# Optimization experiments

Hardware: AMD Instinct MI355X
Metric: run time of the kernel (lower is better)

The kernel has to match this reference:

```python
import jax, jax.numpy as jnp
import numpy as np

B, K, C, HEADS, R, N, FF = 8, 512, 256, 8, 4, 64, 1024
HT = 2 * R + 1  # rel-pos table side = 9


def layer_norm(x, g, b, eps=1e-5):
    mu = jnp.mean(x, axis=-1, keepdims=True)
    var = jnp.var(x, axis=-1, keepdims=True)
    return (x - mu) * jax.lax.rsqrt(var + eps) * g + b


def grid_sample_table(table, grid):
    """Bilinear grid_sample, align_corners=True, zeros padding.
    table: [heads, H, W] (batch-expanded in torch, identical per batch)
    grid:  [b, k, n, 2] in [-1, 1]  ->  out [b, heads, k, n]
    """
    heads, H, W = table.shape
    gx = (grid[..., 0] + 1.0) * 0.5 * (W - 1)
    gy = (grid[..., 1] + 1.0) * 0.5 * (H - 1)
    x0 = jnp.floor(gx); y0 = jnp.floor(gy)
    x1 = x0 + 1.0;      y1 = y0 + 1.0
    wx1 = gx - x0; wx0 = 1.0 - wx1
    wy1 = gy - y0; wy0 = 1.0 - wy1
    flat = table.reshape(heads, H * W)

    def corner(yi, xi, w):
        valid = (xi >= 0) & (xi <= W - 1) & (yi >= 0) & (yi <= H - 1)
        idx = (jnp.clip(yi, 0, H - 1) * W + jnp.clip(xi, 0, W - 1)).astype(jnp.int32)
        return flat[:, idx] * jnp.where(valid, w, 0.0)[None]  # [heads,b,k,n]

    out = (corner(y0, x0, wy0 * wx0) + corner(y0, x1, wy0 * wx1)
           + corner(y1, x0, wy1 * wx0) + corner(y1, x1, wy1 * wx1))
    return jnp.moveaxis(out, 0, 1)  # [b, heads, k, n]


def setup_inputs() -> dict:
    key = jax.random.key(0)
    ks = jax.random.split(key, 16)
    s = 1.0 / np.sqrt(C)
    inp = {
        "query": jax.random.normal(ks[0], (B, K, C), jnp.float32),
        "local_feat": jax.random.normal(ks[1], (B, C, K, N), jnp.float32),
        "local_spat": jax.random.uniform(ks[2], (B, K, N, 2), jnp.float32) * 2.0 - 1.0,
        # rel-pos table is zeros-initialized in torch; use small randn so it's non-trivial
        "rel_table": jax.random.normal(ks[3], (HEADS, HT, HT), jnp.float32) * 0.02,
        "Wq": jax.random.normal(ks[4], (C, C), jnp.float32) * s,
        "bq": jnp.zeros((C,), jnp.float32),
        "Wk": jax.random.normal(ks[5], (C, C), jnp.float32) * s,
        "bk": jnp.zeros((C,), jnp.float32),
        "Wv": jax.random.normal(ks[6], (C, C), jnp.float32) * s,
        "bv": jnp.zeros((C,), jnp.float32),
        "Wo": jax.random.normal(ks[7], (C, C), jnp.float32) * s,
        "bo": jnp.zeros((C,), jnp.float32),
        "ln1_g": jnp.ones((C,), jnp.float32),
        "ln1_b": jnp.zeros((C,), jnp.float32),
        "W1": jax.random.normal(ks[8], (C, FF), jnp.float32) * s,
        "b1": jnp.zeros((FF,), jnp.float32),
        "W2": jax.random.normal(ks[9], (FF, C), jnp.float32) * (1.0 / np.sqrt(FF)),
        "b2": jnp.zeros((C,), jnp.float32),
        "ln2_g": jnp.ones((C,), jnp.float32),
        "ln2_b": jnp.zeros((C,), jnp.float32),
    }
    return inp


def reference(query, local_feat, local_spat, rel_table, Wq, bq, Wk, bk, Wv, bv,
              Wo, bo, ln1_g, ln1_b, W1, b1, W2, b2, ln2_g, ln2_b):
    b, k, c = query.shape
    heads = rel_table.shape[0]
    d = c // heads
    n = local_feat.shape[-1]
    # spatial_score: grid_sample of rel-pos table at per-key offsets -> attention bias
    bias = grid_sample_table(rel_table, local_spat)      # [b, heads, k, n]
    bias = jnp.transpose(bias, (0, 2, 1, 3))             # [b, k, heads, n]
    # local bilateral attention (query attends to its n local samples)
    q = (query @ Wq + bq).reshape(b, k, heads, d)
    feats = jnp.transpose(local_feat, (0, 2, 3, 1))      # [b, k, n, c]
    Kp = (feats @ Wk + bk).reshape(b, k, n, heads, d)
    Vp = (feats @ Wv + bv).reshape(b, k, n, heads, d)
    scores = jnp.einsum('bkhd,bknhd->bkhn', q, Kp) / jnp.sqrt(jnp.float32(d)) + bias
    attn = jax.nn.softmax(scores, axis=-1)
    ctx = jnp.einsum('bkhn,bknhd->bkhd', attn, Vp).reshape(b, k, c)
    x = layer_norm(query + ctx @ Wo + bo, ln1_g, ln1_b)
    h = jax.nn.gelu(x @ W1 + b1) @ W2 + b2
    out = layer_norm(x + h, ln2_g, ln2_b)
    # num_local_scales == 1: stack+mean over scales is identity
    return out
```

## Files before the change

kernel.cpp:

```cpp
#include <hip/hip_runtime.h>
#include <hip/hip_bf16.h>

typedef __hip_bfloat16 bf16;
typedef __attribute__((ext_vector_type(8))) short short8;
typedef __attribute__((ext_vector_type(4))) float float4_;

#define DEV static __device__ __forceinline__

DEV float blo(unsigned w){ return __uint_as_float(w << 16); }
DEV float bhi(unsigned w){ return __uint_as_float(w & 0xffff0000u); }
DEV unsigned short f2bu(float x){ bf16 h = __float2bfloat16(x); unsigned short u; __builtin_memcpy(&u, &h, 2); return u; }
DEV unsigned pack2(float a, float b){ return (unsigned)f2bu(a) | ((unsigned)f2bu(b) << 16); }

DEV float gelu_tanh(float x){
  float z = 0.7978845608028654f * (x + 0.044715f * x * x * x);
  float th = 2.0f / (1.0f + __expf(-2.0f * z)) - 1.0f;
  return 0.5f * x * (1.0f + th);
}


__global__ __launch_bounds__(256) void k_prep(
    const float* __restrict__ query, const float* __restrict__ Wq,
    const float* __restrict__ Wk, const float* __restrict__ Wv,
    const float* __restrict__ Wo, const float* __restrict__ W1, const float* __restrict__ W2,
    const float* __restrict__ bq,
    bf16* __restrict__ query_bf, bf16* __restrict__ WqkT, float* __restrict__ bias_qk,
    bf16* __restrict__ WvP, bf16* __restrict__ WoT, bf16* __restrict__ W1T, bf16* __restrict__ W2T)
{
  __shared__ ushort ts[64][72];
  __shared__ float wkS[32];
  const int t = threadIdx.x;
  const int bx = blockIdx.x;

  if (bx < 144){
    const float* src; bf16* dst; int ldi, ldo, kt, nt;
    if (bx < 16)      { src = Wo; dst = WoT; ldi = 256;  ldo = 256;  kt = bx & 3;        nt = bx >> 2; }
    else if (bx < 80) { src = W1; dst = W1T; ldi = 1024; ldo = 256;  kt = (bx-16) & 3;   nt = (bx-16) >> 2; }
    else              { src = W2; dst = W2T; ldi = 256;  ldo = 1024; kt = (bx-80) & 15;  nt = (bx-80) >> 4; }
    int k0 = kt * 64, n0 = nt * 64;
    {
      int r = t >> 2, c0 = (t & 3) * 16;
      #pragma unroll
      for (int g = 0; g < 4; g++){
        float4 v = *(const float4*)&src[(size_t)(k0 + r)*ldi + n0 + c0 + g*4];
        ts[r][c0+g*4+0] = f2bu(v.x); ts[r][c0+g*4+1] = f2bu(v.y);
        ts[r][c0+g*4+2] = f2bu(v.z); ts[r][c0+g*4+3] = f2bu(v.w);
      }
    }
    __syncthreads();
    {
      int rr = t >> 2, cc0 = (t & 3) * 16;
      unsigned wbuf[8];
      #pragma unroll
      for (int j = 0; j < 8; j++)
        wbuf[j] = (unsigned)ts[cc0+2*j][rr] | ((unsigned)ts[cc0+2*j+1][rr] << 16);
      uint4* d = (uint4*)(dst + (size_t)(n0 + rr)*ldo + k0 + cc0);
      d[0] = make_uint4(wbuf[0], wbuf[1], wbuf[2], wbuf[3]);
      d[1] = make_uint4(wbuf[4], wbuf[5], wbuf[6], wbuf[7]);
    }
  } else if (bx < 176){
    int idx = bx - 144, h = idx >> 2, kt = idx & 3, k0 = kt * 64;
    {
      int r = t >> 2, d0 = (t & 3) * 8;
      #pragma unroll
      for (int g = 0; g < 2; g++){
        float4 v = *(const float4*)&Wv[(size_t)(k0 + r)*256 + h*32 + d0 + g*4];
        ts[r][d0+g*4+0] = f2bu(v.x); ts[r][d0+g*4+1] = f2bu(v.y);
        ts[r][d0+g*4+2] = f2bu(v.z); ts[r][d0+g*4+3] = f2bu(v.w);
      }
    }
    __syncthreads();
    {
      int d = t >> 3, cc0 = (t & 7) * 8;
      unsigned wbuf[4];
      #pragma unroll
      for (int j = 0; j < 4; j++)
        wbuf[j] = (unsigned)ts[cc0+2*j][d] | ((unsigned)ts[cc0+2*j+1][d] << 16);
      *(uint4*)(WvP + (size_t)h*8192 + (size_t)d*256 + k0 + cc0) =
          make_uint4(wbuf[0], wbuf[1], wbuf[2], wbuf[3]);
    }
  } else if (bx < 240){
    int off = (bx - 176) * 16384;
    #pragma unroll
    for (int g = 0; g < 16; g++){
      int i = off + g*1024 + t*4;
      float4 v = *(const float4*)&query[i];
      *(uint2*)(query_bf + i) = make_uint2(pack2(v.x, v.y), pack2(v.z, v.w));
    }
  } else {
    int idx = bx - 240, h = idx >> 8, c = idx & 255;
    if (t < 32) wkS[t] = Wk[(size_t)c*256 + h*32 + t];
    __syncthreads();
    float acc = 0.f;
    const float* wq = Wq + (size_t)t*256 + h*32;
    #pragma unroll
    for (int d = 0; d < 32; d++) acc += wq[d] * wkS[d];
    WqkT[(size_t)(h*256 + c)*256 + t] = __float2bfloat16(acc);
    if (t == 0){
      float bacc = 0.f;
      #pragma unroll
      for (int d = 0; d < 32; d++) bacc += bq[h*32 + d] * wkS[d];
      bias_qk[h*256 + c] = bacc;
    }
  }
}

template<int KDIM, int NT, int EPI>
__global__ __launch_bounds__(256) void k_gemm(
    const bf16* __restrict__ A, int lda, int acolH,
    const bf16* __restrict__ BT, int btH,
    const float* __restrict__ bias,
    bf16* __restrict__ Cb, int ldc, int ncolH)
{
  constexpr int KB = (KDIM >= 64) ? 64 : 32;
  constexpr int LP = KB + 8;
  constexpr int ASEG = KB / 8;
  __shared__ short As[64][LP];
  __shared__ short Bs[NT][LP];

  const int t = threadIdx.x;
  const int w = t >> 6, l = t & 63, lm = l & 15, lq = l >> 4;
  const int m0 = blockIdx.x * 64;
  const int h = blockIdx.z;
  const size_t acol = (size_t)h * acolH;
  const bf16* Bt = BT + (size_t)h * btH + (size_t)(blockIdx.y * NT) * KDIM;
  const int ncol = h * ncolH + blockIdx.y * NT;

  float4_ acc[NT/16];
  #pragma unroll
  for (int i = 0; i < NT/16; i++) acc[i] = (float4_){0.f,0.f,0.f,0.f};

  for (int k0 = 0; k0 < KDIM; k0 += KB){
    if (k0) __syncthreads();
    for (int i = t; i < 64*ASEG; i += 256){
      int row = i / ASEG, seg = i % ASEG;
      uint4 v = *(const uint4*)(A + (size_t)(m0+row)*lda + acol + k0 + seg*8);
      *(uint4*)&As[row][seg*8] = v;
    }
    for (int i = t; i < NT*ASEG; i += 256){
      int row = i / ASEG, seg = i % ASEG;
      uint4 v = *(const uint4*)(Bt + (size_t)row*KDIM + k0 + seg*8);
      *(uint4*)&Bs[row][seg*8] = v;
    }
    __syncthreads();
    #pragma unroll
    for (int kk = 0; kk < KB/32; kk++){
      short8 af = *(const short8*)&As[w*16 + lm][kk*32 + lq*8];
      #pragma unroll
      for (int nt = 0; nt < NT/16; nt++){
        short8 bfr = *(const short8*)&Bs[nt*16 + lm][kk*32 + lq*8];
        acc[nt] = __builtin_amdgcn_mfma_f32_16x16x32_bf16(af, bfr, acc[nt], 0, 0, 0);
      }
    }
  }

  #pragma unroll
  for (int nt = 0; nt < NT/16; nt++){
    int gcol = ncol + nt*16 + lm;
    float bb = bias ? bias[gcol] : 0.0f;
    #pragma unroll
    for (int rg = 0; rg < 4; rg++){
      int row = m0 + w*16 + lq*4 + rg;
      float v = acc[nt][rg] + bb;
      if (EPI == 0) Cb[(size_t)row*ldc + gcol] = __float2bfloat16(v);
      else          Cb[(size_t)row*ldc + gcol] = __float2bfloat16(gelu_tanh(v));
    }
  }
}

template<int KDIM, int WRITE_BF>
__global__ __launch_bounds__(256) void k_gemm_ln(
    const bf16* __restrict__ A, int lda,
    const bf16* __restrict__ BT,
    const float* __restrict__ bias,
    const float* __restrict__ resid,
    const float* __restrict__ gamma, const float* __restrict__ beta,
    float* __restrict__ Cf, bf16* __restrict__ Cb)
{
  constexpr int KB = 64, LP = 72;
  __shared__ short As[16][LP];
  __shared__ short Bs[256][LP];
  __shared__ float2 part[4][16];

  const int t = threadIdx.x;
  const int w = t >> 6, l = t & 63, lm = l & 15, lq = l >> 4;
  const int m0 = blockIdx.x * 16;

  float4_ acc[4];
  #pragma unroll
  for (int i = 0; i < 4; i++) acc[i] = (float4_){0.f,0.f,0.f,0.f};

  for (int k0 = 0; k0 < KDIM; k0 += KB){
    if (k0) __syncthreads();
    if (t < 128){
      int row = t >> 3, seg = t & 7;
      uint4 v = *(const uint4*)(A + (size_t)(m0+row)*lda + k0 + seg*8);
      *(uint4*)&As[row][seg*8] = v;
    }
    for (int i = t; i < 2048; i += 256){
      int row = i >> 3, seg = i & 7;
      uint4 v = *(const uint4*)(BT + (size_t)row*KDIM + k0 + seg*8);
      *(uint4*)&Bs[row][seg*8] = v;
    }
    __syncthreads();
    #pragma unroll
    for (int kk = 0; kk < 2; kk++){
      short8 af = *(const short8*)&As[lm][kk*32 + lq*8];
      #pragma unroll
      for (int nt = 0; nt < 4; nt++){
        short8 bfr = *(const short8*)&Bs[w*64 + nt*16 + lm][kk*32 + lq*8];
        acc[nt] = __builtin_amdgcn_mfma_f32_16x16x32_bf16(af, bfr, acc[nt], 0, 0, 0);
      }
    }
  }

  float v[4][4];
  float s1[4] = {0,0,0,0}, s2[4] = {0,0,0,0};
  #pragma unroll
  for (int nt = 0; nt < 4; nt++){
    int col = w*64 + nt*16 + lm;
    float bb = bias[col];
    #pragma unroll
    for (int rg = 0; rg < 4; rg++){
      int row = m0 + lq*4 + rg;
      float x = acc[nt][rg] + bb + resid[(size_t)row*256 + col];
      v[nt][rg] = x;
      s1[rg] += x; s2[rg] += x*x;
    }
  }
  #pragma unroll
  for (int off = 1; off < 16; off <<= 1){
    #pragma unroll
    for (int rg = 0; rg < 4; rg++){
      s1[rg] += __shfl_xor(s1[rg], off);
      s2[rg] += __shfl_xor(s2[rg], off);
    }
  }
  if (lm == 0){
    #pragma unroll
    for (int rg = 0; rg < 4; rg++)
      part[w][lq*4 + rg] = make_float2(s1[rg], s2[rg]);
  }
  __syncthreads();
  #pragma unroll
  for (int rg = 0; rg < 4; rg++){
    int rl = lq*4 + rg;
    float S1 = part[0][rl].x + part[1][rl].x + part[2][rl].x + part[3][rl].x;
    float S2 = part[0][rl].y + part[1][rl].y + part[2][rl].y + part[3][rl].y;
    float mean = S1 * (1.0f/256.0f);
    float var  = S2 * (1.0f/256.0f) - mean*mean;
    float inv  = rsqrtf(var + 1e-5f);
    #pragma unroll
    for (int nt = 0; nt < 4; nt++){
      int col = w*64 + nt*16 + lm;
      float o = (v[nt][rg] - mean) * inv * gamma[col] + beta[col];
      size_t idx = (size_t)(m0 + rl)*256 + col;
      Cf[idx] = o;
      if (WRITE_BF) Cb[idx] = __float2bfloat16(o);
    }
  }
}

__global__ __launch_bounds__(256) void k_attn(
    const float* __restrict__ local_feat, const float* __restrict__ local_spat,
    const float* __restrict__ rel_table, const bf16* __restrict__ qk,
    bf16* __restrict__ fctx)
{
  __shared__ __attribute__((aligned(16))) ushort fsT[64][256];
  __shared__ __attribute__((aligned(16))) ushort fs[256][64];
  __shared__ __attribute__((aligned(16))) ushort qkb[8][272];
  __shared__ __attribute__((aligned(16))) ushort attnT[16][64];
  __shared__ __attribute__((aligned(16))) float biasS[8][68];
  __shared__ __attribute__((aligned(16))) float s_scT[8][68];

  const int t = threadIdx.x;
  const int r = blockIdx.x;
  const int b = r >> 9, k = r & 511;
  const int w = t >> 6, l = t & 63, lm = l & 15, lq = l >> 4;

  {
    const int cpair = t >> 3;
    const int mrow  = t & 7;
    const int nq8   = mrow * 8;
    #pragma unroll
    for (int p = 0; p < 4; p++){
      int c0 = p*64 + cpair*2, c1 = c0 + 1;
      const float* s0 = local_feat + ((size_t)((b*256 + c0)*512 + k))*64 + nq8;
      const float* s1 = local_feat + ((size_t)((b*256 + c1)*512 + k))*64 + nq8;
      float4 a0 = *(const float4*)(s0);
      float4 a1 = *(const float4*)(s0 + 4);
      float4 b0 = *(const float4*)(s1);
      float4 b1 = *(const float4*)(s1 + 4);
      ushort u0[8] = { f2bu(a0.x), f2bu(a0.y), f2bu(a0.z), f2bu(a0.w),
                       f2bu(a1.x), f2bu(a1.y), f2bu(a1.z), f2bu(a1.w) };
      ushort u1[8] = { f2bu(b0.x), f2bu(b0.y), f2bu(b0.z), f2bu(b0.w),
                       f2bu(b1.x), f2bu(b1.y), f2bu(b1.z), f2bu(b1.w) };
      {
        int sw0 = nq8 ^ ((c0 & 7) << 3);
        int sw1 = nq8 ^ ((c1 & 7) << 3);
        *(uint4*)&fs[c0][sw0] = make_uint4(
            (unsigned)u0[0] | ((unsigned)u0[1]<<16), (unsigned)u0[2] | ((unsigned)u0[3]<<16),
            (unsigned)u0[4] | ((unsigned)u0[5]<<16), (unsigned)u0[6] | ((unsigned)u0[7]<<16));
        *(uint4*)&fs[c1][sw1] = make_uint4(
            (unsigned)u1[0] | ((unsigned)u1[1]<<16), (unsigned)u1[2] | ((unsigned)u1[3]<<16),
            (unsigned)u1[4] | ((unsigned)u1[5]<<16), (unsigned)u1[6] | ((unsigned)u1[7]<<16));
      }
      #pragma unroll
      for (int i = 0; i < 8; i++){
        int key = ((mrow ^ i) & 7) << 3;
        *(unsigned*)&fsT[nq8 + i][c0 ^ key] = (unsigned)u0[i] | ((unsigned)u1[i] << 16);
      }
    }
  }
  {
    uint4 a = *(const uint4*)(qk + (size_t)r * 2048 + t * 8);
    int h = t >> 5, c0 = (t & 31) * 8;
    *(uint4*)&qkb[h][c0] = a;
  }
  if (t < 64){
    float2 sxy = *(const float2*)&local_spat[((size_t)r*64 + t)*2];
    float gx = (sxy.x + 1.0f) * 4.0f, gy = (sxy.y + 1.0f) * 4.0f;
    float x0f = floorf(gx), y0f = floorf(gy);
    int xi0 = (int)x0f, yi0 = (int)y0f;
    float wx1 = gx - x0f, wx0 = 1.0f - wx1;
    float wy1 = gy - y0f, wy0 = 1.0f - wy1;
    int xs[4] = {xi0, xi0 + 1, xi0, xi0 + 1};
    int ys[4] = {yi0, yi0, yi0 + 1, yi0 + 1};
    float wj[4] = {wy0*wx0, wy0*wx1, wy1*wx0, wy1*wx1};
    float ww[4]; int ix[4];
    #pragma unroll
    for (int j = 0; j < 4; j++){
      bool valid = (xs[j] >= 0) && (xs[j] <= 8) && (ys[j] >= 0) && (ys[j] <= 8);
      ix[j] = min(max(ys[j],0),8)*9 + min(max(xs[j],0),8);
      ww[j] = valid ? wj[j] : 0.0f;
    }
    #pragma unroll
    for (int h = 0; h < 8; h++){
      const float* th = rel_table + h*81;
      biasS[h][t] = th[ix[0]]*ww[0] + th[ix[1]]*ww[1] + th[ix[2]]*ww[2] + th[ix[3]]*ww[3];
    }
  }
  __syncthreads();

  {
    float4_ acc = (float4_){0.f,0.f,0.f,0.f};
    const int arow = w*16 + lm;
    const int akey = (((arow >> 3) ^ arow) & 7) << 3;
    #pragma unroll
    for (int ks = 0; ks < 8; ks++){
      short8 af  = *(const short8*)&fsT[arow][(ks*32 + lq*8) ^ akey];
      short8 bfr = *(const short8*)&qkb[lm & 7][ks*32 + lq*8];
      acc = __builtin_amdgcn_mfma_f32_16x16x32_bf16(af, bfr, acc, 0, 0, 0);
    }
    if (lm < 8){
      const float scale = 0.17677669529663687f;
      int n0 = w*16 + lq*4;
      float4 sv;
      sv.x = acc[0]*scale + biasS[lm][n0+0];
      sv.y = acc[1]*scale + biasS[lm][n0+1];
      sv.z = acc[2]*scale + biasS[lm][n0+2];
      sv.w = acc[3]*scale + biasS[lm][n0+3];
      *(float4*)&s_scT[lm][n0] = sv;
    }
  }
  __syncthreads();

  {
    int g = t >> 5, j = t & 31;
    float sc0 = s_scT[g][j], sc1 = s_scT[g][j+32];
    float m = fmaxf(sc0, sc1);
    #pragma unroll
    for (int off = 1; off < 32; off <<= 1) m = fmaxf(m, __shfl_xor(m, off));
    float e0 = __expf(sc0 - m), e1 = __expf(sc1 - m);
    float s = e0 + e1;
    #pragma unroll
    for (int off = 1; off < 32; off <<= 1) s += __shfl_xor(s, off);
    float inv = 1.0f / s;
    ushort p0 = f2bu(e0 * inv), p1 = f2bu(e1 * inv);
    int key = g << 3;
    attnT[g    ][j        ^ key] = p0;
    attnT[g    ][(j + 32) ^ key] = p1;
    attnT[g + 8][j        ^ key] = p0;
    attnT[g + 8][(j + 32) ^ key] = p1;
  }
  __syncthreads();

  {
    const int bkey = (lm & 7) << 3;
    short8 bf0 = *(const short8*)&attnT[lm][(      lq*8) ^ bkey];
    short8 bf1 = *(const short8*)&attnT[lm][(32 + lq*8) ^ bkey];
    #pragma unroll
    for (int ct = 0; ct < 4; ct++){
      int crow = (w*4 + ct)*16 + lm;
      int ckey = (crow & 7) << 3;
      float4_ acc2 = (float4_){0.f,0.f,0.f,0.f};
      short8 af0 = *(const short8*)&fs[crow][(      lq*8) ^ ckey];
      acc2 = __builtin_amdgcn_mfma_f32_16x16x32_bf16(af0, bf0, acc2, 0, 0, 0);
      short8 af1 = *(const short8*)&fs[crow][(32 + lq*8) ^ ckey];
      acc2 = __builtin_amdgcn_mfma_f32_16x16x32_bf16(af1, bf1, acc2, 0, 0, 0);
      if (lm < 8){
        int c = (w*4 + ct)*16 + lq*4;
        size_t base = (size_t)r*2048 + (size_t)lm*256 + c;
        *(uint2*)&fctx[base] = make_uint2(pack2(acc2[0], acc2[1]), pack2(acc2[2], acc2[3]));
      }
    }
  }
}

extern "C" void kernel_launch(void* const* d_in, const int* in_sizes, int n_in,
                              void* d_out, int out_size, void* d_ws, size_t ws_size,
                              hipStream_t stream)
{
  const float* query      = (const float*)d_in[0];
  const float* local_feat = (const float*)d_in[1];
  const float* local_spat = (const float*)d_in[2];
  const float* rel_table  = (const float*)d_in[3];
  const float* Wq  = (const float*)d_in[4];   const float* bq  = (const float*)d_in[5];
  const float* Wk  = (const float*)d_in[6];
  const float* Wv  = (const float*)d_in[8];   const float* bv  = (const float*)d_in[9];
  const float* Wo  = (const float*)d_in[10];  const float* bo  = (const float*)d_in[11];
  const float* g1  = (const float*)d_in[12];  const float* be1 = (const float*)d_in[13];
  const float* W1  = (const float*)d_in[14];  const float* b1  = (const float*)d_in[15];
  const float* W2  = (const float*)d_in[16];  const float* b2  = (const float*)d_in[17];
  const float* g2  = (const float*)d_in[18];  const float* be2 = (const float*)d_in[19];

  char* ws = (char*)d_ws;
  bf16*  qk       = (bf16*)(ws + 0);
  bf16*  fctx     = (bf16*)(ws + 16777216);
  bf16*  query_bf = (bf16*)(ws + 33554432);
  bf16*  WqkT     = (bf16*)(ws + 35651584);
  bf16*  WoT      = (bf16*)(ws + 36700160);
  bf16*  WvP      = (bf16*)(ws + 36831232);
  bf16*  W1T      = (bf16*)(ws + 36962304);
  bf16*  W2T      = (bf16*)(ws + 37486592);
  float* bias_qk  = (float*)(ws + 38010880);
  bf16*  ctx_bf   = (bf16*)(ws + 0);
  float* x        = (float*)(ws + 2097152);
  bf16*  x_bf     = (bf16*)(ws + 6291456);
  bf16*  h1       = (bf16*)(ws + 20971520);
  float* out      = (float*)d_out;

  dim3 blk(256);
  k_prep<<<dim3(2288), blk, 0, stream>>>(query, Wq, Wk, Wv, Wo, W1, W2, bq,
                                         query_bf, WqkT, bias_qk, WvP, WoT, W1T, W2T);
  k_gemm<256,64,0><<<dim3(64,32,1), blk, 0, stream>>>(query_bf, 256, 0, WqkT, 0, bias_qk, qk, 2048, 0);
  k_attn<<<dim3(4096), blk, 0, stream>>>(local_feat, local_spat, rel_table, qk, fctx);
  k_gemm<256,32,0><<<dim3(64,1,8), blk, 0, stream>>>(fctx, 2048, 256, WvP, 8192, bv, ctx_bf, 256, 32);
  k_gemm_ln<256,1><<<dim3(256), blk, 0, stream>>>(ctx_bf, 256, WoT, bo, query, g1, be1, x, x_bf);
  k_gemm<256,64,2><<<dim3(64,16,1), blk, 0, stream>>>(x_bf, 256, 0, W1T, 0, b1, h1, 1024, 0);
  k_gemm_ln<1024,0><<<dim3(256), blk, 0, stream>>>(h1, 1024, W2T, b2, x, g2, be2, out, nullptr);
}
```

Measured before the change: 506.0 us.

## Double-buffer shared memory with register prefetch in the GEMM kernels

```diff
diff --git a/kernel.cpp b/kernel.cpp
--- a/kernel.cpp
+++ b/kernel.cpp
@@ -112,11 +112,14 @@
     const float* __restrict__ bias,
     bf16* __restrict__ Cb, int ldc, int ncolH)
 {
-  constexpr int KB = (KDIM >= 64) ? 64 : 32;
+  constexpr int KB = 64;
   constexpr int LP = KB + 8;
   constexpr int ASEG = KB / 8;
-  __shared__ short As[64][LP];
-  __shared__ short Bs[NT][LP];
+  constexpr int NKS = KDIM / KB;
+  constexpr int AIT = (64*ASEG)/256;
+  constexpr int BIT = (NT*ASEG)/256;
+  __shared__ short As[2][64][LP];
+  __shared__ short Bs[2][NT][LP];
 
   const int t = threadIdx.x;
   const int w = t >> 6, l = t & 63, lm = l & 15, lq = l >> 4;
@@ -130,27 +133,50 @@
   #pragma unroll
   for (int i = 0; i < NT/16; i++) acc[i] = (float4_){0.f,0.f,0.f,0.f};
 
-  for (int k0 = 0; k0 < KDIM; k0 += KB){
-    if (k0) __syncthreads();
-    for (int i = t; i < 64*ASEG; i += 256){
-      int row = i / ASEG, seg = i % ASEG;
-      uint4 v = *(const uint4*)(A + (size_t)(m0+row)*lda + acol + k0 + seg*8);
-      *(uint4*)&As[row][seg*8] = v;
-    }
-    for (int i = t; i < NT*ASEG; i += 256){
-      int row = i / ASEG, seg = i % ASEG;
-      uint4 v = *(const uint4*)(Bt + (size_t)row*KDIM + k0 + seg*8);
-      *(uint4*)&Bs[row][seg*8] = v;
-    }
-    __syncthreads();
+  uint4 ra[AIT], rb[BIT];
+  auto loadAB = [&](int k0){
+    #pragma unroll
+    for (int j = 0; j < AIT; j++){
+      int i = t + j*256, row = i / ASEG, seg = i % ASEG;
+      ra[j] = *(const uint4*)(A + (size_t)(m0+row)*lda + acol + k0 + seg*8);
+    }
+    #pragma unroll
+    for (int j = 0; j < BIT; j++){
+      int i = t + j*256, row = i / ASEG, seg = i % ASEG;
+      rb[j] = *(const uint4*)(Bt + (size_t)row*KDIM + k0 + seg*8);
+    }
+  };
+  auto storeAB = [&](int buf){
+    #pragma unroll
+    for (int j = 0; j < AIT; j++){
+      int i = t + j*256, row = i / ASEG, seg = i % ASEG;
+      *(uint4*)&As[buf][row][seg*8] = ra[j];
+    }
+    #pragma unroll
+    for (int j = 0; j < BIT; j++){
+      int i = t + j*256, row = i / ASEG, seg = i % ASEG;
+      *(uint4*)&Bs[buf][row][seg*8] = rb[j];
+    }
+  };
+
+  loadAB(0);
+  storeAB(0);
+  __syncthreads();
+  for (int ks = 0; ks < NKS; ks++){
+    int cur = ks & 1;
+    if (ks + 1 < NKS) loadAB((ks+1)*KB);
     #pragma unroll
     for (int kk = 0; kk < KB/32; kk++){
-      short8 af = *(const short8*)&As[w*16 + lm][kk*32 + lq*8];
+      short8 af = *(const short8*)&As[cur][w*16 + lm][kk*32 + lq*8];
       #pragma unroll
       for (int nt = 0; nt < NT/16; nt++){
-        short8 bfr = *(const short8*)&Bs[nt*16 + lm][kk*32 + lq*8];
+        short8 bfr = *(const short8*)&Bs[cur][nt*16 + lm][kk*32 + lq*8];
         acc[nt] = __builtin_amdgcn_mfma_f32_16x16x32_bf16(af, bfr, acc[nt], 0, 0, 0);
       }
+    }
+    if (ks + 1 < NKS){
+      storeAB(cur ^ 1);
+      __syncthreads();
     }
   }
 
@@ -178,8 +204,9 @@
     float* __restrict__ Cf, bf16* __restrict__ Cb)
 {
   constexpr int KB = 64, LP = 72;
-  __shared__ short As[16][LP];
-  __shared__ short Bs[256][LP];
+  constexpr int NKS = KDIM / KB;
+  __shared__ short As[2][16][LP];
+  __shared__ short Bs[2][256][LP];
   __shared__ float2 part[4][16];
 
   const int t = threadIdx.x;
@@ -190,27 +217,49 @@
   #pragma unroll
   for (int i = 0; i < 4; i++) acc[i] = (float4_){0.f,0.f,0.f,0.f};
 
-  for (int k0 = 0; k0 < KDIM; k0 += KB){
-    if (k0) __syncthreads();
+  uint4 ra;
+  uint4 rb[8];
+  auto loadAB = [&](int k0){
     if (t < 128){
       int row = t >> 3, seg = t & 7;
-      uint4 v = *(const uint4*)(A + (size_t)(m0+row)*lda + k0 + seg*8);
-      *(uint4*)&As[row][seg*8] = v;
-    }
-    for (int i = t; i < 2048; i += 256){
-      int row = i >> 3, seg = i & 7;
-      uint4 v = *(const uint4*)(BT + (size_t)row*KDIM + k0 + seg*8);
-      *(uint4*)&Bs[row][seg*8] = v;
-    }
-    __syncthreads();
+      ra = *(const uint4*)(A + (size_t)(m0+row)*lda + k0 + seg*8);
+    }
+    #pragma unroll
+    for (int j = 0; j < 8; j++){
+      int i = t + j*256, row = i >> 3, seg = i & 7;
+      rb[j] = *(const uint4*)(BT + (size_t)row*KDIM + k0 + seg*8);
+    }
+  };
+  auto storeAB = [&](int buf){
+    if (t < 128){
+      int row = t >> 3, seg = t & 7;
+      *(uint4*)&As[buf][row][seg*8] = ra;
+    }
+    #pragma unroll
+    for (int j = 0; j < 8; j++){
+      int i = t + j*256, row = i >> 3, seg = i & 7;
+      *(uint4*)&Bs[buf][row][seg*8] = rb[j];
+    }
+  };
+
+  loadAB(0);
+  storeAB(0);
+  __syncthreads();
+  for (int ks = 0; ks < NKS; ks++){
+    int cur = ks & 1;
+    if (ks + 1 < NKS) loadAB((ks+1)*KB);
     #pragma unroll
     for (int kk = 0; kk < 2; kk++){
-      short8 af = *(const short8*)&As[lm][kk*32 + lq*8];
+      short8 af = *(const short8*)&As[cur][lm][kk*32 + lq*8];
       #pragma unroll
       for (int nt = 0; nt < 4; nt++){
-        short8 bfr = *(const short8*)&Bs[w*64 + nt*16 + lm][kk*32 + lq*8];
+        short8 bfr = *(const short8*)&Bs[cur][w*64 + nt*16 + lm][kk*32 + lq*8];
         acc[nt] = __builtin_amdgcn_mfma_f32_16x16x32_bf16(af, bfr, acc[nt], 0, 0, 0);
       }
+    }
+    if (ks + 1 < NKS){
+      storeAB(cur ^ 1);
+      __syncthreads();
     }
   }
 
```

Measured after the change: 538.6 us. 1.06x slower.
